# Kernel tuning notes

Measured on AMD Instinct MI355X. Metric: run time of the kernel, lower is better.

## Reference

```python
import jax, jax.numpy as jnp
import numpy as np

HIDDEN = 1024
HEADS = 16
HEAD_DIM = HIDDEN // HEADS
SCALE = float(np.sqrt(HEAD_DIM))


def setup_inputs() -> dict:
    key = jax.random.key(0)
    ks = jax.random.split(key, 5)
    x = jax.random.normal(ks[0], (2, 2048, HIDDEN), dtype=jnp.float32)
    # qkv_proj: Linear(hidden, 3*hidden); torch stores weight as [out, in]
    w_qkv = jax.random.normal(ks[1], (3 * HIDDEN, HIDDEN), dtype=jnp.float32) / np.sqrt(HIDDEN)
    b_qkv = jax.random.normal(ks[2], (3 * HIDDEN,), dtype=jnp.float32) * 0.02
    w_out = jax.random.normal(ks[3], (HIDDEN, HIDDEN), dtype=jnp.float32) / np.sqrt(HIDDEN)
    b_out = jax.random.normal(ks[4], (HIDDEN,), dtype=jnp.float32) * 0.02
    return {"x": x, "w_qkv": w_qkv, "b_qkv": b_qkv, "w_out": w_out, "b_out": b_out}


def reference(x, w_qkv, b_qkv, w_out, b_out):
    B, S, H = x.shape
    # fused QKV projection -> [B, S, 3, heads, head_dim]
    qkv = (jnp.einsum('bsh,oh->bso', x, w_qkv) + b_qkv).reshape(B, S, 3, HEADS, HEAD_DIM)
    q, k, v = qkv[:, :, 0], qkv[:, :, 1], qkv[:, :, 2]
    scores = jnp.einsum('bqhd,bkhd->bhqk', q, k) / SCALE
    attn = jax.nn.softmax(scores, axis=-1)  # dropout p=0.0 (eval)
    ctx = jnp.einsum('bhqk,bkhd->bqhd', attn, v).reshape(B, S, H)
    return jnp.einsum('bsh,oh->bso', ctx, w_out) + b_out
```

## Files before the change

### kernel.cpp

```cpp
#include <hip/hip_runtime.h>
#include <math.h>

#define BATCH 2
#define SEQ   2048
#define HIDDEN 1024
#define HEADS 16
#define HD    64
#define QSCALE 0.18033688011112042f

typedef __attribute__((ext_vector_type(8)))  short short8;
typedef __attribute__((ext_vector_type(16))) float f32x16;

__device__ __forceinline__ unsigned short f2bf(float f) {
    unsigned int u = __builtin_bit_cast(unsigned int, f);
    u = (u + 0x7FFFu + ((u >> 16) & 1u)) >> 16;
    return (unsigned short)u;
}
__device__ __forceinline__ unsigned int cvt_pk_bf16(float lo, float hi) {
    unsigned int r;
    asm("v_cvt_pk_bf16_f32 %0, %1, %2" : "=v"(r) : "v"(lo), "v"(hi));
    return r;
}
__device__ __forceinline__ void gl16(const void* g, void* l) {
    __builtin_amdgcn_global_load_lds(
        (const __attribute__((address_space(1))) void*)g,
        (__attribute__((address_space(3))) void*)l,
        16, 0, 0);
}
#define WAIT_VM(N) asm volatile("s_waitcnt vmcnt(" #N ")" ::: "memory")
#define BARRIER()  do { __builtin_amdgcn_s_barrier(); __builtin_amdgcn_sched_barrier(0); } while (0)

__global__ __launch_bounds__(256)
void conv_all(const float* __restrict__ x,  unsigned short* __restrict__ xh,
              const float* __restrict__ wq, unsigned short* __restrict__ wqh,
              const float* __restrict__ wo, unsigned short* __restrict__ woh)
{
    int b = blockIdx.x;
    const float* src;
    unsigned short* dst;
    int base;
    if (b < 4096)      { src = x;  dst = xh;  base = b; }
    else if (b < 7168) { src = wq; dst = wqh; base = b - 4096; }
    else               { src = wo; dst = woh; base = b - 7168; }
    int idx = base * 256 + threadIdx.x;
    float4 v = ((const float4*)src)[idx];
    ushort4 h4;
    h4.x = f2bf(v.x); h4.y = f2bf(v.y); h4.z = f2bf(v.z); h4.w = f2bf(v.w);
    ((ushort4*)dst)[idx] = h4;
}

__device__ __forceinline__ void gemm_core1(
    const char* Ah, const char* Bh,
    int m0, int n0, char* smem, f32x16 acc[2][2])
{
    const int t    = threadIdx.x;
    const int lane = t & 63;
    const int w    = t >> 6;
    const int wm   = w >> 1, wn = w & 1;
    const int l31  = lane & 31, hh = lane >> 5;

    auto stage = [&](int buf, int kt) {
        #pragma unroll
        for (int i = 0; i < 2; ++i) {
            int r  = i * 64 + (t >> 2);
            int cs = (t & 3) ^ ((r >> 1) & 3);
            gl16(Ah + ((size_t)(m0 + r) * 1024 + kt * 32 + cs * 8) * 2,
                 smem + buf * 16384 + i * 4096 + w * 1024);
            gl16(Bh + ((size_t)(n0 + r) * 1024 + kt * 32 + cs * 8) * 2,
                 smem + buf * 16384 + 8192 + i * 4096 + w * 1024);
        }
    };

    stage(0, 0);
    int cur = 0, nxt = 1;
    for (int kt = 0; kt < 32; ++kt) {
        if (kt + 1 < 32) {
            stage(nxt, kt + 1);
            WAIT_VM(4);
        } else {
            WAIT_VM(0);
        }
        BARRIER();
        const char* Ab = smem + cur * 16384;
        const char* Bb = Ab + 8192;
        #pragma unroll
        for (int ks = 0; ks < 2; ++ks) {
            short8 ah[2], bh[2];
            #pragma unroll
            for (int mt = 0; mt < 2; ++mt) {
                int R  = wm * 64 + mt * 32 + l31;
                int ch = ((ks * 2 + hh) ^ ((R >> 1) & 3)) * 16;
                ah[mt] = *(const short8*)(Ab + R * 64 + ch);
            }
            #pragma unroll
            for (int nt = 0; nt < 2; ++nt) {
                int R  = wn * 64 + nt * 32 + l31;
                int ch = ((ks * 2 + hh) ^ ((R >> 1) & 3)) * 16;
                bh[nt] = *(const short8*)(Bb + R * 64 + ch);
            }
            #pragma unroll
            for (int mt = 0; mt < 2; ++mt)
                #pragma unroll
                for (int nt = 0; nt < 2; ++nt)
                    acc[mt][nt] = __builtin_amdgcn_mfma_f32_32x32x16_bf16(ah[mt], bh[nt], acc[mt][nt], 0, 0, 0);
        }
        cur = nxt;
        nxt = (nxt == 2) ? 0 : nxt + 1;
    }
    __syncthreads();
}

__global__ __launch_bounds__(256, 3)
void qkv_gemm(const unsigned short* __restrict__ xh,
              const unsigned short* __restrict__ wh,
              const float* __restrict__ bias,
              unsigned short* __restrict__ qB, unsigned short* __restrict__ kB,
              unsigned short* __restrict__ vtB)
{
    __shared__ __align__(16) char smem[49152];
    f32x16 acc[2][2] = {{{}, {}}, {{}, {}}};
    const int m0 = blockIdx.x * 128, n0 = blockIdx.y * 128;
    gemm_core1((const char*)xh, (const char*)wh, m0, n0, smem, acc);

    const int t    = threadIdx.x;
    const int lane = t & 63;
    const int w    = t >> 6;
    const int wm   = w >> 1, wn = w & 1;
    const int l31  = lane & 31, hh = lane >> 5;

    const int which = n0 >> 10;
    const float scl = (which == 0) ? QSCALE : 1.0f;

    #pragma unroll
    for (int mt = 0; mt < 2; ++mt)
        #pragma unroll
        for (int nt = 0; nt < 2; ++nt) {
            int nl = wn * 64 + nt * 32 + l31;
            float bb = bias[n0 + nl];
            #pragma unroll
            for (int r = 0; r < 16; ++r) {
                int ml = wm * 64 + mt * 32 + (r & 3) + 8 * (r >> 2) + 4 * hh;
                float val = (acc[mt][nt][r] + bb) * scl;
                *(unsigned short*)(smem + ml * 272 + nl * 2) = f2bf(val);
            }
        }
    __syncthreads();

    const int hbase = (n0 & 1023) >> 6;
    const int b     = m0 >> 11;
    const int s0    = m0 & 2047;

    if (which < 2) {
        unsigned short* pp = which ? kB : qB;
        const int nc   = t & 31;
        const int head = hbase + (nc >> 4);
        const int d0   = (nc & 15) * 4;
        #pragma unroll
        for (int it = 0; it < 16; ++it) {
            int m = it * 8 + (t >> 5);
            ushort4 h4 = *(const ushort4*)(smem + m * 272 + nc * 8);
            size_t idx = (((size_t)(b * HEADS + head)) * SEQ + s0 + m) * HD + d0;
            *(ushort4*)&pp[idx] = h4;
        }
    } else {
        const int nl   = t & 127;
        const int head = hbase + (nl >> 6);
        const int d    = nl & 63;
        #pragma unroll
        for (int it = 0; it < 16; ++it) {
            int mq = it * 2 + (t >> 7);
            ushort4 h4;
            h4.x = *(const unsigned short*)(smem + (mq * 4 + 0) * 272 + nl * 2);
            h4.y = *(const unsigned short*)(smem + (mq * 4 + 1) * 272 + nl * 2);
            h4.z = *(const unsigned short*)(smem + (mq * 4 + 2) * 272 + nl * 2);
            h4.w = *(const unsigned short*)(smem + (mq * 4 + 3) * 272 + nl * 2);
            size_t idx = (((size_t)(b * HEADS + head)) * HD + d) * SEQ + s0 + mq * 4;
            *(ushort4*)&vtB[idx] = h4;
        }
    }
}

__global__ __launch_bounds__(256, 3)
void out_gemm(const unsigned short* __restrict__ cth,
              const unsigned short* __restrict__ bh_,
              const float* __restrict__ bias, float* __restrict__ out)
{
    __shared__ __align__(16) char smem[49152];
    f32x16 acc[2][2] = {{{}, {}}, {{}, {}}};
    const int m0 = blockIdx.x * 128, n0 = blockIdx.y * 128;
    gemm_core1((const char*)cth, (const char*)bh_, m0, n0, smem, acc);

    const int t    = threadIdx.x;
    const int lane = t & 63;
    const int w    = t >> 6;
    const int wm   = w >> 1, wn = w & 1;
    const int l31  = lane & 31, hh = lane >> 5;

    #pragma unroll
    for (int mt = 0; mt < 2; ++mt)
        #pragma unroll
        for (int nt = 0; nt < 2; ++nt) {
            int n = n0 + wn * 64 + nt * 32 + l31;
            float bb = bias[n];
            #pragma unroll
            for (int r = 0; r < 16; ++r) {
                int m = m0 + wm * 64 + mt * 32 + (r & 3) + 8 * (r >> 2) + 4 * hh;
                out[(size_t)m * 1024 + n] = acc[mt][nt][r] + bb;
            }
        }
}

#define NPAIR (SEQ / 64)

__global__ __launch_bounds__(256, 2)
void attn_mfma(const unsigned short* __restrict__ qB, const unsigned short* __restrict__ kB,
               const unsigned short* __restrict__ vtB, unsigned short* __restrict__ ctxb)
{
    __shared__ __align__(16) char smem[65536];
    const int t    = threadIdx.x;
    const int lane = t & 63;
    const int wq   = t >> 6;
    const int l31  = lane & 31;
    const int hh   = lane >> 5;

    const int bid = blockIdx.x;
    const int xcd = bid & 7, j = bid >> 3;
    const int qt  = j & 15;
    const int bhg = xcd + 8 * (j >> 4);
    const int q0  = qt * 128;
    const size_t bh = (size_t)bhg;

    const char* qP = (const char*)(qB + bh * SEQ * HD);
    const char* kP = (const char*)(kB + bh * SEQ * HD);
    const char* vP = (const char*)(vtB + bh * SEQ * HD);

    const int wbase = wq * 1024;

    {
        int rr = t >> 3, cc = t & 7;
        #pragma unroll
        for (int i = 0; i < 4; ++i) {
            int row = i * 32 + rr;
            int ch  = cc ^ (row & 7);
            gl16(qP + (size_t)(q0 + row) * 128 + ch * 16, smem + i * 4096 + wbase);
        }
    }
    auto stagePair = [&](int p) {
        int base = ((p + 1) & 3) * 16384;
        int rr = t >> 3;
        int ch = (t & 7) ^ (rr & 7);
        gl16(kP + (size_t)(p * 64 + rr) * 128 + ch * 16,      smem + base +     0 + wbase);
        gl16(kP + (size_t)(p * 64 + 32 + rr) * 128 + ch * 16, smem + base +  4096 + wbase);
        int rr2 = t >> 2;
        int s4  = (rr2 & 3) ^ ((rr2 >> 2) & 3);
        int ch2 = (t & 3) ^ s4;
        gl16(vP + (size_t)rr2 * (SEQ * 2) + p * 128 +      ch2 * 16, smem + base +  8192 + wbase);
        gl16(vP + (size_t)rr2 * (SEQ * 2) + p * 128 + 64 + ch2 * 16, smem + base + 12288 + wbase);
    };
    stagePair(0);
    stagePair(1);
    WAIT_VM(8);
    BARRIER();

    short8 qf[4];
    {
        int qrow = 32 * wq + l31;
        #pragma unroll
        for (int ks = 0; ks < 4; ++ks) {
            int ch = ((2 * ks + hh) ^ (qrow & 7)) * 16;
            qf[ks] = *(const short8*)(smem + qrow * 128 + ch);
        }
    }
    asm volatile("s_waitcnt lgkmcnt(0)" ::: "memory");
    __builtin_amdgcn_sched_barrier(0);
    WAIT_VM(4);
    BARRIER();

    f32x16 sa = {}, sb = {};
    {
        const char* Pb = smem + 16384;
        __builtin_amdgcn_s_setprio(1);
        #pragma unroll
        for (int ks = 0; ks < 4; ++ks) {
            int ch = ((2 * ks + hh) ^ (l31 & 7)) * 16;
            short8 ka = *(const short8*)(Pb +        l31 * 128 + ch);
            short8 kb = *(const short8*)(Pb + 4096 + l31 * 128 + ch);
            sa = __builtin_amdgcn_mfma_f32_32x32x16_bf16(ka, qf[ks], sa, 0, 0, 0);
            sb = __builtin_amdgcn_mfma_f32_32x32x16_bf16(kb, qf[ks], sb, 0, 0, 0);
        }
        __builtin_amdgcn_s_setprio(0);
    }

    f32x16 acc0 = {}, acc1 = {};
    float lsum = 0.0f;

    for (int i = 0; i < NPAIR; ++i) {
        if (i + 2 < NPAIR) { stagePair(i + 2); WAIT_VM(4); }
        else if (i + 1 < NPAIR) { WAIT_VM(0); }
        BARRIER();

        f32x16 na = {}, nb = {};
        if (i + 1 < NPAIR) {
            const char* Pn = smem + ((i + 2) & 3) * 16384;
            __builtin_amdgcn_s_setprio(1);
            #pragma unroll
            for (int ks = 0; ks < 4; ++ks) {
                int ch = ((2 * ks + hh) ^ (l31 & 7)) * 16;
                short8 ka = *(const short8*)(Pn +        l31 * 128 + ch);
                short8 kb = *(const short8*)(Pn + 4096 + l31 * 128 + ch);
                na = __builtin_amdgcn_mfma_f32_32x32x16_bf16(ka, qf[ks], na, 0, 0, 0);
                nb = __builtin_amdgcn_mfma_f32_32x32x16_bf16(kb, qf[ks], nb, 0, 0, 0);
            }
            __builtin_amdgcn_s_setprio(0);
        }

        unsigned int pa_[8], pb_[8];
        float ps0 = 0.f, ps1 = 0.f, ps2 = 0.f, ps3 = 0.f;
        #pragma unroll
        for (int w = 0; w < 8; ++w) {
            float e0 = __builtin_amdgcn_exp2f(sa[2 * w]);
            float e1 = __builtin_amdgcn_exp2f(sa[2 * w + 1]);
            ps0 += e0; ps1 += e1;
            pa_[w] = cvt_pk_bf16(e0, e1);
            float f0 = __builtin_amdgcn_exp2f(sb[2 * w]);
            float f1 = __builtin_amdgcn_exp2f(sb[2 * w + 1]);
            ps2 += f0; ps3 += f1;
            pb_[w] = cvt_pk_bf16(f0, f1);
        }
        lsum += (ps0 + ps1) + (ps2 + ps3);

        const char* Pb = smem + ((i + 1) & 3) * 16384;
        const char* Va = Pb + 8192;
        const char* Vb = Pb + 12288;
        __builtin_amdgcn_s_setprio(1);
        #pragma unroll
        for (int ks = 0; ks < 2; ++ks) {
            unsigned int a0 = pa_[4*ks],     a2 = pa_[4*ks + 2];
            unsigned int a1 = pa_[4*ks + 1], a3 = pa_[4*ks + 3];
            asm volatile("v_permlane32_swap_b32 %0, %1" : "+v"(a0), "+v"(a2));
            asm volatile("v_permlane32_swap_b32 %0, %1" : "+v"(a1), "+v"(a3));
            unsigned int b0 = pb_[4*ks],     b2 = pb_[4*ks + 2];
            unsigned int b1 = pb_[4*ks + 1], b3 = pb_[4*ks + 3];
            asm volatile("v_permlane32_swap_b32 %0, %1" : "+v"(b0), "+v"(b2));
            asm volatile("v_permlane32_swap_b32 %0, %1" : "+v"(b1), "+v"(b3));
            short8 pA = __builtin_bit_cast(short8, make_uint4(a0, a1, a2, a3));
            short8 pB = __builtin_bit_cast(short8, make_uint4(b0, b1, b2, b3));
            #pragma unroll
            for (int mt = 0; mt < 2; ++mt) {
                int rrow = 32 * mt + l31;
                int s4   = (rrow & 3) ^ ((rrow >> 2) & 3);
                int ch   = ((2 * ks + hh) ^ s4) * 16;
                short8 va = *(const short8*)(Va + rrow * 64 + ch);
                short8 vb = *(const short8*)(Vb + rrow * 64 + ch);
                if (mt == 0) {
                    acc0 = __builtin_amdgcn_mfma_f32_32x32x16_bf16(va, pA, acc0, 0, 0, 0);
                    acc0 = __builtin_amdgcn_mfma_f32_32x32x16_bf16(vb, pB, acc0, 0, 0, 0);
                } else {
                    acc1 = __builtin_amdgcn_mfma_f32_32x32x16_bf16(va, pA, acc1, 0, 0, 0);
                    acc1 = __builtin_amdgcn_mfma_f32_32x32x16_bf16(vb, pB, acc1, 0, 0, 0);
                }
            }
        }
        __builtin_amdgcn_s_setprio(0);

        sa = na; sb = nb;
    }

    lsum += __shfl_xor(lsum, 32, 64);
    __syncthreads();
    float inv = 1.0f / lsum;
    {
        int q = 32 * wq + l31;
        #pragma unroll
        for (int mt = 0; mt < 2; ++mt) {
            #pragma unroll
            for (int m2 = 0; m2 < 4; ++m2) {
                ushort4 h4;
                if (mt == 0) {
                    h4.x = f2bf(acc0[4*m2+0] * inv); h4.y = f2bf(acc0[4*m2+1] * inv);
                    h4.z = f2bf(acc0[4*m2+2] * inv); h4.w = f2bf(acc0[4*m2+3] * inv);
                } else {
                    h4.x = f2bf(acc1[4*m2+0] * inv); h4.y = f2bf(acc1[4*m2+1] * inv);
                    h4.z = f2bf(acc1[4*m2+2] * inv); h4.w = f2bf(acc1[4*m2+3] * inv);
                }
                int d0 = 4 * hh + 8 * m2 + 32 * mt;
                int c  = (d0 >> 3) ^ (q & 7);
                *(ushort4*)(smem + q * 128 + c * 16 + (d0 & 7) * 2) = h4;
            }
        }
    }
    __syncthreads();
    {
        #pragma unroll
        for (int it = 0; it < 4; ++it) {
            int slot = it * 256 + t;
            int row  = slot >> 3;
            int p    = slot & 7;
            uint4 v4 = *(const uint4*)(smem + row * 128 + ((p ^ (row & 7)) * 16));
            *(uint4*)&ctxb[((size_t)(bhg >> 4) * SEQ + q0 + row) * HIDDEN
                           + (bhg & 15) * HD + p * 8] = v4;
        }
    }
}

extern "C" void kernel_launch(void* const* d_in, const int* in_sizes, int n_in,
                              void* d_out, int out_size, void* d_ws, size_t ws_size,
                              hipStream_t stream)
{
    const float* x     = (const float*)d_in[0];
    const float* w_qkv = (const float*)d_in[1];
    const float* b_qkv = (const float*)d_in[2];
    const float* w_out = (const float*)d_in[3];
    const float* b_out = (const float*)d_in[4];
    float* out = (float*)d_out;

    const size_t PH = (size_t)BATCH * HEADS * SEQ * HD;
    unsigned short* ws = (unsigned short*)d_ws;
    unsigned short* qB  = ws;
    unsigned short* kB  = ws + PH;
    unsigned short* vtB = ws + 2 * PH;
    unsigned short* wqh = ws + 3 * PH;
    unsigned short* woh = wqh + 3 * PH / 4;
    unsigned short* cth = woh + PH / 4;
    unsigned short* xh  = (unsigned short*)d_out;

    conv_all<<<8192, 256, 0, stream>>>(x, xh, w_qkv, wqh, w_out, woh);
    qkv_gemm<<<dim3(32, 24), 256, 0, stream>>>(xh, wqh, b_qkv, qB, kB, vtB);
    attn_mfma<<<512, 256, 0, stream>>>(qB, kB, vtB, cth);
    out_gemm<<<dim3(32, 8), 256, 0, stream>>>(cth, woh, b_out, out);
}
```

Measured before the change: 110.6 us.

## Split attention KV range across two wave groups per block and merge partials

Each attention block now runs 512 threads as two groups of four waves, each processing half of the key/value sequence with its own double-buffered LDS ring. Partial accumulators and row sums from the second group are written to shared memory and merged by the first group before normalisation and store. This targets low per-CU wave occupancy on the serial KV loop. In exchange, the prefetch depth drops from two pairs ahead to one, S-compute is no longer overlapped with the PV step, and an extra barrier per iteration plus a merge pass through LDS are added.

Result: faster. 107.8 us (median of 2 runs) (-2.6%).

```diff
diff --git a/kernel.cpp b/kernel.cpp
--- a/kernel.cpp
+++ b/kernel.cpp
@@ -212,14 +212,16 @@
 
 #define NPAIR (SEQ / 64)
 
-__global__ __launch_bounds__(256, 2)
+__global__ __launch_bounds__(512, 4)
 void attn_mfma(const unsigned short* __restrict__ qB, const unsigned short* __restrict__ kB,
                const unsigned short* __restrict__ vtB, unsigned short* __restrict__ ctxb)
 {
-    __shared__ __align__(16) char smem[65536];
+    __shared__ __align__(16) char smem[66048];
     const int t    = threadIdx.x;
     const int lane = t & 63;
     const int wq   = t >> 6;
+    const int grp  = wq >> 2;
+    const int wql  = wq & 3;
     const int l31  = lane & 31;
     const int hh   = lane >> 5;
 
@@ -234,51 +236,61 @@
     const char* kP = (const char*)(kB + bh * SEQ * HD);
     const char* vP = (const char*)(vtB + bh * SEQ * HD);
 
-    const int wbase = wq * 1024;
+    const int ringb = grp * 32768;
+    const int wb    = wql * 1024;
+    const int tg    = t & 255;
 
     {
         int rr = t >> 3, cc = t & 7;
         #pragma unroll
-        for (int i = 0; i < 4; ++i) {
-            int row = i * 32 + rr;
+        for (int i = 0; i < 2; ++i) {
+            int row = i * 64 + rr;
             int ch  = cc ^ (row & 7);
-            gl16(qP + (size_t)(q0 + row) * 128 + ch * 16, smem + i * 4096 + wbase);
-        }
-    }
-    auto stagePair = [&](int p) {
-        int base = ((p + 1) & 3) * 16384;
-        int rr = t >> 3;
-        int ch = (t & 7) ^ (rr & 7);
-        gl16(kP + (size_t)(p * 64 + rr) * 128 + ch * 16,      smem + base +     0 + wbase);
-        gl16(kP + (size_t)(p * 64 + 32 + rr) * 128 + ch * 16, smem + base +  4096 + wbase);
-        int rr2 = t >> 2;
+            gl16(qP + (size_t)(q0 + row) * 128 + ch * 16,
+                 smem + 49152 + i * 8192 + wq * 1024);
+        }
+    }
+    auto stageP = [&](int buf, int p) {
+        int base = ringb + buf * 16384;
+        int rr = tg >> 3;
+        int ch = (tg & 7) ^ (rr & 7);
+        gl16(kP + (size_t)(p * 64 + rr) * 128 + ch * 16,      smem + base +     0 + wb);
+        gl16(kP + (size_t)(p * 64 + 32 + rr) * 128 + ch * 16, smem + base +  4096 + wb);
+        int rr2 = tg >> 2;
         int s4  = (rr2 & 3) ^ ((rr2 >> 2) & 3);
-        int ch2 = (t & 3) ^ s4;
-        gl16(vP + (size_t)rr2 * (SEQ * 2) + p * 128 +      ch2 * 16, smem + base +  8192 + wbase);
-        gl16(vP + (size_t)rr2 * (SEQ * 2) + p * 128 + 64 + ch2 * 16, smem + base + 12288 + wbase);
+        int ch2 = (tg & 3) ^ s4;
+        gl16(vP + (size_t)rr2 * (SEQ * 2) + p * 128 +      ch2 * 16, smem + base +  8192 + wb);
+        gl16(vP + (size_t)rr2 * (SEQ * 2) + p * 128 + 64 + ch2 * 16, smem + base + 12288 + wb);
     };
-    stagePair(0);
-    stagePair(1);
-    WAIT_VM(8);
+    const int p0 = grp * (NPAIR / 2);
+    stageP(0, p0);
+    WAIT_VM(4);
     BARRIER();
 
     short8 qf[4];
     {
-        int qrow = 32 * wq + l31;
+        int qrow = 32 * wql + l31;
         #pragma unroll
         for (int ks = 0; ks < 4; ++ks) {
             int ch = ((2 * ks + hh) ^ (qrow & 7)) * 16;
-            qf[ks] = *(const short8*)(smem + qrow * 128 + ch);
+            qf[ks] = *(const short8*)(smem + 49152 + qrow * 128 + ch);
         }
     }
     asm volatile("s_waitcnt lgkmcnt(0)" ::: "memory");
     __builtin_amdgcn_sched_barrier(0);
-    WAIT_VM(4);
     BARRIER();
 
-    f32x16 sa = {}, sb = {};
-    {
-        const char* Pb = smem + 16384;
+    f32x16 acc0 = {}, acc1 = {};
+    float lsum = 0.0f;
+
+    for (int i = 0; i < NPAIR / 2; ++i) {
+        if (i + 1 < NPAIR / 2) { stageP((i + 1) & 1, p0 + i + 1); WAIT_VM(4); }
+        else                   { WAIT_VM(0); }
+        BARRIER();
+
+        const char* Pb = smem + ringb + (i & 1) * 16384;
+
+        f32x16 sa = {}, sb = {};
         __builtin_amdgcn_s_setprio(1);
         #pragma unroll
         for (int ks = 0; ks < 4; ++ks) {
@@ -289,30 +301,6 @@
             sb = __builtin_amdgcn_mfma_f32_32x32x16_bf16(kb, qf[ks], sb, 0, 0, 0);
         }
         __builtin_amdgcn_s_setprio(0);
-    }
-
-    f32x16 acc0 = {}, acc1 = {};
-    float lsum = 0.0f;
-
-    for (int i = 0; i < NPAIR; ++i) {
-        if (i + 2 < NPAIR) { stagePair(i + 2); WAIT_VM(4); }
-        else if (i + 1 < NPAIR) { WAIT_VM(0); }
-        BARRIER();
-
-        f32x16 na = {}, nb = {};
-        if (i + 1 < NPAIR) {
-            const char* Pn = smem + ((i + 2) & 3) * 16384;
-            __builtin_amdgcn_s_setprio(1);
-            #pragma unroll
-            for (int ks = 0; ks < 4; ++ks) {
-                int ch = ((2 * ks + hh) ^ (l31 & 7)) * 16;
-                short8 ka = *(const short8*)(Pn +        l31 * 128 + ch);
-                short8 kb = *(const short8*)(Pn + 4096 + l31 * 128 + ch);
-                na = __builtin_amdgcn_mfma_f32_32x32x16_bf16(ka, qf[ks], na, 0, 0, 0);
-                nb = __builtin_amdgcn_mfma_f32_32x32x16_bf16(kb, qf[ks], nb, 0, 0, 0);
-            }
-            __builtin_amdgcn_s_setprio(0);
-        }
 
         unsigned int pa_[8], pb_[8];
         float ps0 = 0.f, ps1 = 0.f, ps2 = 0.f, ps3 = 0.f;
@@ -329,7 +317,6 @@
         }
         lsum += (ps0 + ps1) + (ps2 + ps3);
 
-        const char* Pb = smem + ((i + 1) & 3) * 16384;
         const char* Va = Pb + 8192;
         const char* Vb = Pb + 12288;
         __builtin_amdgcn_s_setprio(1);
@@ -362,38 +349,53 @@
             }
         }
         __builtin_amdgcn_s_setprio(0);
-
-        sa = na; sb = nb;
+        BARRIER();
     }
 
     lsum += __shfl_xor(lsum, 32, 64);
     __syncthreads();
-    float inv = 1.0f / lsum;
-    {
-        int q = 32 * wq + l31;
-        #pragma unroll
-        for (int mt = 0; mt < 2; ++mt) {
-            #pragma unroll
-            for (int m2 = 0; m2 < 4; ++m2) {
-                ushort4 h4;
-                if (mt == 0) {
-                    h4.x = f2bf(acc0[4*m2+0] * inv); h4.y = f2bf(acc0[4*m2+1] * inv);
-                    h4.z = f2bf(acc0[4*m2+2] * inv); h4.w = f2bf(acc0[4*m2+3] * inv);
-                } else {
-                    h4.x = f2bf(acc1[4*m2+0] * inv); h4.y = f2bf(acc1[4*m2+1] * inv);
-                    h4.z = f2bf(acc1[4*m2+2] * inv); h4.w = f2bf(acc1[4*m2+3] * inv);
-                }
-                int d0 = 4 * hh + 8 * m2 + 32 * mt;
-                int c  = (d0 >> 3) ^ (q & 7);
-                *(ushort4*)(smem + q * 128 + c * 16 + (d0 & 7) * 2) = h4;
-            }
+    const int qrow = 32 * wql + l31;
+    if (grp == 1) {
+        int idx = t - 256;
+        #pragma unroll
+        for (int m2 = 0; m2 < 4; ++m2) {
+            *(float4*)(smem + 16384 + (m2 * 256 + idx) * 16) =
+                make_float4(acc0[4*m2+0], acc0[4*m2+1], acc0[4*m2+2], acc0[4*m2+3]);
+            *(float4*)(smem + 16384 + ((m2 + 4) * 256 + idx) * 16) =
+                make_float4(acc1[4*m2+0], acc1[4*m2+1], acc1[4*m2+2], acc1[4*m2+3]);
+        }
+        if (hh == 0) ((float*)(smem + 65536))[qrow] = lsum;
+    }
+    __syncthreads();
+    if (grp == 0) {
+        float l1 = ((float*)(smem + 65536))[qrow];
+        float inv = 1.0f / (lsum + l1);
+        #pragma unroll
+        for (int m2 = 0; m2 < 4; ++m2) {
+            float4 pa = *(const float4*)(smem + 16384 + (m2 * 256 + t) * 16);
+            float4 pb = *(const float4*)(smem + 16384 + ((m2 + 4) * 256 + t) * 16);
+            ushort4 h4a, h4b;
+            h4a.x = f2bf((acc0[4*m2+0] + pa.x) * inv);
+            h4a.y = f2bf((acc0[4*m2+1] + pa.y) * inv);
+            h4a.z = f2bf((acc0[4*m2+2] + pa.z) * inv);
+            h4a.w = f2bf((acc0[4*m2+3] + pa.w) * inv);
+            h4b.x = f2bf((acc1[4*m2+0] + pb.x) * inv);
+            h4b.y = f2bf((acc1[4*m2+1] + pb.y) * inv);
+            h4b.z = f2bf((acc1[4*m2+2] + pb.z) * inv);
+            h4b.w = f2bf((acc1[4*m2+3] + pb.w) * inv);
+            int d0a = 4 * hh + 8 * m2;
+            int ca  = (d0a >> 3) ^ (qrow & 7);
+            *(ushort4*)(smem + qrow * 128 + ca * 16 + (d0a & 7) * 2) = h4a;
+            int d0b = 4 * hh + 8 * m2 + 32;
+            int cb  = (d0b >> 3) ^ (qrow & 7);
+            *(ushort4*)(smem + qrow * 128 + cb * 16 + (d0b & 7) * 2) = h4b;
         }
     }
     __syncthreads();
     {
         #pragma unroll
-        for (int it = 0; it < 4; ++it) {
-            int slot = it * 256 + t;
+        for (int it = 0; it < 2; ++it) {
+            int slot = it * 512 + t;
             int row  = slot >> 3;
             int p    = slot & 7;
             uint4 v4 = *(const uint4*)(smem + row * 128 + ((p ^ (row & 7)) * 16));
@@ -426,6 +428,6 @@
 
     conv_all<<<8192, 256, 0, stream>>>(x, xh, w_qkv, wqh, w_out, woh);
     qkv_gemm<<<dim3(32, 24), 256, 0, stream>>>(xh, wqh, b_qkv, qB, kB, vtB);
-    attn_mfma<<<512, 256, 0, stream>>>(qB, kB, vtB, cth);
+    attn_mfma<<<512, 512, 0, stream>>>(qB, kB, vtB, cth);
     out_gemm<<<dim3(32, 8), 256, 0, stream>>>(cth, woh, b_out, out);
 }
```
